# Kernel optimization log

Hardware: AMD Instinct MI355X
Metric: run time of the kernel (lower is better)

The kernel has to match this reference:

```python
import jax, jax.numpy as jnp
import numpy as np

VOCAB = 1024
EMBED_DIM = 64
COMMIT_COST = 0.25


def setup_inputs() -> dict:
    key = jax.random.key(0)
    k1, k2 = jax.random.split(key)
    z_e = jax.random.normal(k1, (64, 64, 32, 32), dtype=jnp.float32)
    # nn.Embedding init: uniform(-1/vocab, 1/vocab)
    embedding = jax.random.uniform(
        k2, (VOCAB, EMBED_DIM), dtype=jnp.float32,
        minval=-1.0 / VOCAB, maxval=1.0 / VOCAB)
    return {"z_e": z_e, "embedding": embedding}


def reference(z_e, embedding):
    b, d, h, w = z_e.shape
    # [B,D,H,W] -> [N,D]
    flat_z = jnp.transpose(z_e, (0, 2, 3, 1)).reshape(-1, d)
    # squared L2 distances to each code: [N, V]
    distances = (
        jnp.sum(flat_z * flat_z, axis=1, keepdims=True)
        + jnp.sum(embedding * embedding, axis=1)
        - 2.0 * flat_z @ embedding.T
    )
    flat_indices = jnp.argmin(distances, axis=1)
    indices = flat_indices.reshape(b, h, w)
    # gather codes and restore [B,D,H,W]
    z_q = embedding[flat_indices].reshape(b, h, w, d)
    z_q = jnp.transpose(z_q, (0, 3, 1, 2))
    quantization_loss = jnp.mean((z_q - jax.lax.stop_gradient(z_e)) ** 2)
    commitment_loss = jnp.mean((z_e - jax.lax.stop_gradient(z_q)) ** 2) * COMMIT_COST
    z_q_st = z_e + jax.lax.stop_gradient(z_q - z_e)
    # perplexity over codebook usage
    counts = jnp.zeros((VOCAB,), dtype=jnp.float32).at[flat_indices].add(1.0)
    avg_probs = counts / flat_indices.shape[0]
    perplexity = jnp.exp(-jnp.sum(avg_probs * jnp.log(avg_probs + 1e-10)))
    return (z_q_st, indices, quantization_loss, commitment_loss, perplexity)
```

## Files before the change

### kernel.cpp

```cpp
#include <hip/hip_runtime.h>
#include <math.h>

#define VOCAB 1024
#define ED 64
#define NROWS 65536
#define NELEM 4194304
#define MARGIN 2.0e-4f
#define CAPF 8192

typedef __attribute__((ext_vector_type(8))) short short8;
typedef __attribute__((ext_vector_type(4))) float f32x4;

__device__ __forceinline__ unsigned f2bf(float f) {
    unsigned u = __float_as_uint(f);
    u += 0x7fff + ((u >> 16) & 1);
    return u >> 16;
}

__device__ __forceinline__ unsigned long long packkey(float d, int c) {
    unsigned f = __float_as_uint(d);
    unsigned sd = (f & 0x80000000u) ? ~f : (f | 0x80000000u);
    return ((unsigned long long)sd << 32) | (unsigned)c;
}


__global__ void vq_prep(const float* __restrict__ emb, float* __restrict__ e2f,
                        uint4* __restrict__ FB, unsigned* __restrict__ zw1,
                        unsigned* __restrict__ zw2) {
    const int tid = blockIdx.x * 256 + threadIdx.x;
    for (int i = tid; i < 1028; i += 2048) zw1[i] = 0u;
    for (int i = tid; i < 3072; i += 2048) zw2[i] = 0u;

    if (tid < VOCAB) {
        const float4* src = (const float4*)(emb + tid * ED);
        double s = 0.0;
        #pragma unroll
        for (int g = 0; g < 16; ++g) {
            float4 f = src[g];
            s = fma((double)f.x, (double)f.x, s);
            s = fma((double)f.y, (double)f.y, s);
            s = fma((double)f.z, (double)f.z, s);
            s = fma((double)f.w, (double)f.w, s);
        }
        e2f[tid] = (float)s;
    }
    #pragma unroll
    for (int e = 0; e < 4; ++e) {
        const int i = e * 2048 + tid;
        const int n = i & 15, q = (i >> 4) & 3, kh = (i >> 6) & 1, T = i >> 7;
        const int code = T * 16 + n;
        const int k0 = kh * 32 + q * 8;
        const float4* sp = (const float4*)(emb + code * 64 + k0);
        float4 f0 = sp[0], f1 = sp[1];
        uint4 pk;
        pk.x = f2bf(f0.x) | (f2bf(f0.y) << 16);
        pk.y = f2bf(f0.z) | (f2bf(f0.w) << 16);
        pk.z = f2bf(f1.x) | (f2bf(f1.y) << 16);
        pk.w = f2bf(f1.z) | (f2bf(f1.w) << 16);
        FB[i] = pk;
    }
}

__global__ __launch_bounds__(256, 2)
void vq_filter(const float* __restrict__ z, const float* __restrict__ emb,
               const float* __restrict__ e2f, const uint4* __restrict__ FB,
               float* __restrict__ out, double* __restrict__ lossp,
               unsigned* __restrict__ hist, unsigned* __restrict__ nflag,
               unsigned* __restrict__ rowlist, float* __restrict__ zrow) {
    __shared__ uint4 Bs4[4096];
    __shared__ float e2s[1024];
    __shared__ float rowb1[128], rowb2[128];
    __shared__ int   rowi1[128], rowfl[128];
    __shared__ double wls[4];

    const int t = threadIdx.x;
    const int w = t >> 6, lane = t & 63;
    const int q = lane >> 4, n_lo = lane & 15;
    const int bk = blockIdx.x;
    const int n0 = bk * 128;
    const int b  = n0 >> 10;
    const int sb = n0 & 1023;

    #pragma unroll
    for (int i = 0; i < 4; ++i) e2s[i * 256 + t] = e2f[i * 256 + t];

    short8 af[2][2];
    #pragma unroll
    for (int rt = 0; rt < 2; ++rt) {
        const int s = sb + w * 32 + rt * 16 + n_lo;
        const float* zp = z + (size_t)b * 65536 + s;
        #pragma unroll
        for (int kh = 0; kh < 2; ++kh) {
            short8 fr;
            #pragma unroll
            for (int j = 0; j < 8; ++j) {
                int d = kh * 32 + q * 8 + j;
                fr[j] = (short)f2bf(-2.0f * zp[d * 1024]);
            }
            af[rt][kh] = fr;
        }
    }

    float b1[8], b2[8]; int i1[8];
    #pragma unroll
    for (int sl = 0; sl < 8; ++sl) { b1[sl] = 3.4e38f; b2[sl] = 3.4e38f; i1[sl] = 0; }

    const short8* FBs = (const short8*)Bs4;
    for (int h = 0; h < 2; ++h) {
        __syncthreads();
        {
            const uint4* src = FB + h * 4096;
            #pragma unroll
            for (int i = 0; i < 16; ++i) Bs4[i * 256 + t] = src[i * 256 + t];
        }
        __syncthreads();
        #pragma unroll 2
        for (int tt = 0; tt < 32; ++tt) {
            const int T = h * 32 + tt;
            short8 bf0 = FBs[tt * 128 + lane];
            short8 bf1 = FBs[tt * 128 + 64 + lane];
            const int cb = T * 16 + n_lo;
            const float e2 = e2s[cb];
            #pragma unroll
            for (int rt = 0; rt < 2; ++rt) {
                f32x4 a; a[0] = e2; a[1] = e2; a[2] = e2; a[3] = e2;
                a = __builtin_amdgcn_mfma_f32_16x16x32_bf16(af[rt][0], bf0, a, 0, 0, 0);
                a = __builtin_amdgcn_mfma_f32_16x16x32_bf16(af[rt][1], bf1, a, 0, 0, 0);
                #pragma unroll
                for (int reg = 0; reg < 4; ++reg) {
                    const int sl = rt * 4 + reg;
                    float s0 = a[reg];
                    b2[sl] = __builtin_amdgcn_fmed3f(s0, b1[sl], b2[sl]);
                    bool lt = s0 < b1[sl];
                    i1[sl] = lt ? cb : i1[sl];
                    b1[sl] = lt ? s0 : b1[sl];
                }
            }
        }
    }

    #pragma unroll
    for (int m = 1; m < 16; m <<= 1) {
        #pragma unroll
        for (int sl = 0; sl < 8; ++sl) {
            float ob1 = __shfl_xor(b1[sl], m, 64);
            int   oi1 = __shfl_xor(i1[sl], m, 64);
            float ob2 = __shfl_xor(b2[sl], m, 64);
            float lose = fmaxf(b1[sl], ob1);
            b2[sl] = fminf(fminf(b2[sl], ob2), lose);
            bool take = (ob1 < b1[sl]) || (ob1 == b1[sl] && oi1 < i1[sl]);
            b1[sl] = take ? ob1 : b1[sl];
            i1[sl] = take ? oi1 : i1[sl];
        }
    }
    if (n_lo == 0) {
        #pragma unroll
        for (int rt = 0; rt < 2; ++rt) {
            #pragma unroll
            for (int reg = 0; reg < 4; ++reg) {
                int row = w * 32 + rt * 16 + q * 4 + reg;
                int sl = rt * 4 + reg;
                rowb1[row] = b1[sl];
                rowb2[row] = b2[sl];
                rowi1[row] = i1[sl];
            }
        }
    }
    __syncthreads();

    if (t < 128) {
        const int nrow = n0 + t;
        const int code = rowi1[t];
        const bool want = rowb2[t] < rowb1[t] + MARGIN;
        unsigned long long mask = __ballot(want);
        const int cnt = __popcll(mask);
        unsigned base = 0;
        if (lane == 0 && cnt > 0) base = atomicAdd(nflag, (unsigned)cnt);
        base = (unsigned)__shfl((int)base, 0, 64);
        int myslot = -1;
        if (want) {
            const int rank = __popcll(mask & ((1ULL << lane) - 1ULL));
            const unsigned slot = base + (unsigned)rank;
            if (slot < CAPF) { rowlist[slot] = (unsigned)nrow; myslot = (int)slot; }
        }
        rowfl[t] = myslot;
        out[NELEM + nrow] = (float)code;
        if (myslot < 0) atomicAdd(&hist[code], 1u);
    }
    __syncthreads();

    {
        const int r = t & 127, tg = t >> 7;
        const int code2 = rowi1[r];
        const int sl2 = rowfl[r];
        const bool fl2 = sl2 >= 0;
        const int scol = sb + r;
        double lsum = 0.0;
        #pragma unroll
        for (int i = 0; i < 8; ++i) {
            const int d4 = tg * 8 + i;
            float4 e4 = *(const float4*)(emb + code2 * 64 + d4 * 4);
            float es[4] = {e4.x, e4.y, e4.z, e4.w};
            #pragma unroll
            for (int j = 0; j < 4; ++j) {
                int d = d4 * 4 + j;
                size_t off = (size_t)b * 65536 + (size_t)d * 1024 + scol;
                float zv = z[off];
                out[off] = zv + (es[j] - zv);
                if (fl2) zrow[(size_t)sl2 * 64 + d] = zv;
                double df = (double)es[j] - (double)zv;
                lsum = fma(df, df, lsum);
            }
        }
        if (fl2) lsum = 0.0;
        #pragma unroll
        for (int off = 32; off > 0; off >>= 1)
            lsum += __shfl_down(lsum, off, 64);
        if (lane == 0) wls[w] = lsum;
    }
    __syncthreads();
    if (t == 0) lossp[bk] = wls[0] + wls[1] + wls[2] + wls[3];
}

#define EDOT(i) { \
    const float4 a4 = za4[i]; \
    const float4 b4 = zb4[i]; \
    ma = fmaf(a4.x, e##i[0], ma); ma = fmaf(a4.y, e##i[1], ma); \
    ma = fmaf(a4.z, e##i[2], ma); ma = fmaf(a4.w, e##i[3], ma); \
    mb = fmaf(b4.x, e##i[0], mb); mb = fmaf(b4.y, e##i[1], mb); \
    mb = fmaf(b4.z, e##i[2], mb); mb = fmaf(b4.w, e##i[3], mb); }

__global__ __launch_bounds__(512, 1)
void vq_rescue(const float* __restrict__ zrow, const float* __restrict__ emb,
               const float* __restrict__ e2f, float* __restrict__ out,
               double* __restrict__ lossp2, unsigned* __restrict__ hist,
               const unsigned* __restrict__ nflag,
               const unsigned* __restrict__ rowlist) {
    __shared__ float zns[16];
    __shared__ unsigned long long wkey[16][16];
    __shared__ int rbi[16];
    __shared__ double lred[8];

    const int t = threadIdx.x, w = t >> 6, lane = t & 63;
    const int g = blockIdx.x;
    unsigned nfr = *nflag;
    const int nf = (int)(nfr < CAPF ? nfr : CAPF);
    if (g * 16 >= nf) return;
    const int nloc = (nf - g * 16 < 16) ? (nf - g * 16) : 16;

    if (t < nloc) {
        const float* zp = zrow + (size_t)(g * 16 + t) * 64;
        double a = 0.0;
        for (int k = 0; k < 64; ++k) { const double v = (double)zp[k]; a = fma(v, v, a); }
        zns[t] = (float)a;
    }
    __syncthreads();

    for (int pass = 0; pass < 2; ++pass) {
        const int cbase = pass * 512 + w * 64;
        const int c = cbase + lane;
        const f32x4* ep = (const f32x4*)(emb + (size_t)c * 64);
        f32x4 e0 = ep[0],  e1 = ep[1],  e2 = ep[2],  e3 = ep[3];
        f32x4 e4 = ep[4],  e5 = ep[5],  e6 = ep[6],  e7 = ep[7];
        f32x4 e8 = ep[8],  e9 = ep[9],  e10 = ep[10], e11 = ep[11];
        f32x4 e12 = ep[12], e13 = ep[13], e14 = ep[14], e15 = ep[15];
        const float e2c = e2f[c];

        for (int r0 = 0; r0 < nloc; r0 += 2) {
            const bool two = (r0 + 1 < nloc);
            const float4* za4 = (const float4*)(zrow + (size_t)(g * 16 + r0) * 64);
            const float4* zb4 = (const float4*)(zrow + (size_t)(g * 16 + (two ? r0 + 1 : r0)) * 64);
            float ma = 0.f, mb = 0.f;
            EDOT(0)  EDOT(1)  EDOT(2)  EDOT(3)
            EDOT(4)  EDOT(5)  EDOT(6)  EDOT(7)
            EDOT(8)  EDOT(9)  EDOT(10) EDOT(11)
            EDOT(12) EDOT(13) EDOT(14) EDOT(15)

            {
                const float da = (zns[r0] + e2c) - 2.0f * ma;
                float dmin = da;
                #pragma unroll
                for (int mo = 32; mo > 0; mo >>= 1)
                    dmin = fminf(dmin, __shfl_xor(dmin, mo, 64));
                const unsigned long long ball = __ballot(da == dmin);
                const int wl = __ffsll(ball) - 1;
                if (lane == 0) wkey[pass * 8 + w][r0] = packkey(dmin, cbase + wl);
            }
            if (two) {
                const float db = (zns[r0 + 1] + e2c) - 2.0f * mb;
                float dmin = db;
                #pragma unroll
                for (int mo = 32; mo > 0; mo >>= 1)
                    dmin = fminf(dmin, __shfl_xor(dmin, mo, 64));
                const unsigned long long ball = __ballot(db == dmin);
                const int wl = __ffsll(ball) - 1;
                if (lane == 0) wkey[pass * 8 + w][r0 + 1] = packkey(dmin, cbase + wl);
            }
        }
    }
    __syncthreads();

    if (t < nloc) {
        unsigned long long k0 = wkey[0][t];
        #pragma unroll
        for (int i = 1; i < 16; ++i) {
            unsigned long long ki = wkey[i][t];
            if (ki < k0) k0 = ki;
        }
        const int code = (int)(unsigned)(k0 & 0xffffffffu);
        rbi[t] = code;
        const int row = (int)rowlist[g * 16 + t];
        out[NELEM + row] = (float)code;
        atomicAdd(&hist[code], 1u);
    }
    __syncthreads();

    double lsum = 0.0;
    if (t < 128) {
        const int r = t >> 3, d0 = (t & 7) * 8;
        if (r < nloc) {
            const int row = (int)rowlist[g * 16 + r];
            const int bb = row >> 10, s = row & 1023;
            const int code = rbi[r];
            float4 ea = *(const float4*)(emb + code * 64 + d0);
            float4 eb = *(const float4*)(emb + code * 64 + d0 + 4);
            float es[8] = {ea.x, ea.y, ea.z, ea.w, eb.x, eb.y, eb.z, eb.w};
            const float* zp = zrow + (size_t)(g * 16 + r) * 64 + d0;
            #pragma unroll
            for (int j = 0; j < 8; ++j) {
                const int d = d0 + j;
                const size_t off = (size_t)bb * 65536 + (size_t)d * 1024 + s;
                const float zv = zp[j];
                out[off] = zv + (es[j] - zv);
                double df = (double)es[j] - (double)zv;
                lsum = fma(df, df, lsum);
            }
        }
    }
    #pragma unroll
    for (int o = 32; o > 0; o >>= 1) lsum += __shfl_down(lsum, o, 64);
    if (lane == 0) lred[w] = lsum;
    __syncthreads();
    if (t == 0) {
        double s = 0.0;
        #pragma unroll
        for (int i = 0; i < 8; ++i) s += lred[i];
        lossp2[g] = s;
    }
}

__global__ void vq_finalize_kernel(const unsigned* __restrict__ hist,
                                   const double* __restrict__ lossp,
                                   const double* __restrict__ lossp2,
                                   float* __restrict__ out) {
    __shared__ double red[256], red2[256];
    int t = threadIdx.x;
    double ssum = 0.0, lsum = 0.0;
    for (int i = t; i < VOCAB; i += 256) {
        double p = (double)hist[i] / (double)NROWS;
        ssum += p * log(p + 1e-10);
    }
    for (int i = t; i < 1024; i += 256) lsum += lossp[i];
    for (int i = t; i < 512; i += 256) lsum += lossp2[i];
    red[t] = ssum; red2[t] = lsum;
    __syncthreads();
    for (int off = 128; off > 0; off >>= 1) {
        if (t < off) { red[t] += red[t + off]; red2[t] += red2[t + off]; }
        __syncthreads();
    }
    if (t == 0) {
        double qv = red2[0] / (double)NELEM;
        out[NELEM + NROWS + 0] = (float)qv;
        out[NELEM + NROWS + 1] = (float)(qv * 0.25);
        out[NELEM + NROWS + 2] = (float)exp(-red[0]);
    }
}

extern "C" void kernel_launch(void* const* d_in, const int* in_sizes, int n_in,
                              void* d_out, int out_size, void* d_ws, size_t ws_size,
                              hipStream_t stream) {
    const float* z   = (const float*)d_in[0];
    const float* emb = (const float*)d_in[1];
    float* out = (float*)d_out;

    float*    e2f     = (float*)d_ws;
    unsigned* nfl     = (unsigned*)((char*)d_ws + 4096);
    unsigned* hist    = (unsigned*)((char*)d_ws + 4112);
    unsigned* rowlist = (unsigned*)((char*)d_ws + 8208);
    uint4*    FB      = (uint4*)((char*)d_ws + 40976);
    double*   lossp   = (double*)((char*)d_ws + 172048);
    double*   lossp2  = (double*)((char*)d_ws + 180240);
    float*    zrow    = (float*)((char*)d_ws + 184336);
    unsigned* zw1     = (unsigned*)((char*)d_ws + 4096);
    unsigned* zw2     = (unsigned*)((char*)d_ws + 172048);

    vq_prep<<<dim3(8), dim3(256), 0, stream>>>(emb, e2f, FB, zw1, zw2);
    vq_filter<<<dim3(512), dim3(256), 0, stream>>>(z, emb, e2f, FB, out, lossp,
                                                   hist, nfl, rowlist, zrow);
    vq_rescue<<<dim3(512), dim3(512), 0, stream>>>(zrow, emb, e2f, out, lossp2,
                                                   hist, nfl, rowlist);
    vq_finalize_kernel<<<dim3(1), dim3(256), 0, stream>>>(hist, lossp, lossp2, out);
}
```

Measured before the change: 158.3 us.

## Split codebook scan across four blocks per row group and merge partial minima

The fused filter kernel is split into two. vq_scan runs 2048 blocks, each scanning a quarter of the codebook for 128 rows, and writes per-row best, second-best and index to workspace. vq_merge then reduces the four partials per row, handles flagging, the histogram, the output write and the loss. This raises parallelism and occupancy, and scan blocks read B fragments straight from global/L2 instead of staging them in LDS. The cost is an extra kernel launch, partial-result traffic, and the z fragments being loaded four times.

```diff
diff --git a/kernel.cpp b/kernel.cpp
--- a/kernel.cpp
+++ b/kernel.cpp
@@ -29,7 +29,7 @@
                         unsigned* __restrict__ zw2) {
     const int tid = blockIdx.x * 256 + threadIdx.x;
     for (int i = tid; i < 1028; i += 2048) zw1[i] = 0u;
-    for (int i = tid; i < 3072; i += 2048) zw2[i] = 0u;
+    for (int i = tid; i < 1536; i += 2048) zw2[i] = 0u;
 
     if (tid < VOCAB) {
         const float4* src = (const float4*)(emb + tid * ED);
@@ -61,28 +61,22 @@
     }
 }
 
-__global__ __launch_bounds__(256, 2)
-void vq_filter(const float* __restrict__ z, const float* __restrict__ emb,
-               const float* __restrict__ e2f, const uint4* __restrict__ FB,
-               float* __restrict__ out, double* __restrict__ lossp,
-               unsigned* __restrict__ hist, unsigned* __restrict__ nflag,
-               unsigned* __restrict__ rowlist, float* __restrict__ zrow) {
-    __shared__ uint4 Bs4[4096];
-    __shared__ float e2s[1024];
-    __shared__ float rowb1[128], rowb2[128];
-    __shared__ int   rowi1[128], rowfl[128];
-    __shared__ double wls[4];
+__global__ __launch_bounds__(256, 4)
+void vq_scan(const float* __restrict__ z, const float* __restrict__ e2f,
+             const uint4* __restrict__ FB, float* __restrict__ pb1,
+             float* __restrict__ pb2, unsigned short* __restrict__ pi1) {
+    __shared__ float e2s[256];
 
     const int t = threadIdx.x;
     const int w = t >> 6, lane = t & 63;
     const int q = lane >> 4, n_lo = lane & 15;
     const int bk = blockIdx.x;
-    const int n0 = bk * 128;
+    const int rg = bk >> 2, ck = bk & 3;
+    const int n0 = rg * 128;
     const int b  = n0 >> 10;
     const int sb = n0 & 1023;
 
-    #pragma unroll
-    for (int i = 0; i < 4; ++i) e2s[i * 256 + t] = e2f[i * 256 + t];
+    if (t < 256) e2s[t] = e2f[ck * 256 + t];
 
     short8 af[2][2];
     #pragma unroll
@@ -105,36 +99,29 @@
     #pragma unroll
     for (int sl = 0; sl < 8; ++sl) { b1[sl] = 3.4e38f; b2[sl] = 3.4e38f; i1[sl] = 0; }
 
-    const short8* FBs = (const short8*)Bs4;
-    for (int h = 0; h < 2; ++h) {
-        __syncthreads();
-        {
-            const uint4* src = FB + h * 4096;
+    __syncthreads();
+
+    const short8* FBs = (const short8*)FB;
+    #pragma unroll 4
+    for (int tt = 0; tt < 16; ++tt) {
+        const int T = ck * 16 + tt;
+        short8 bf0 = FBs[T * 128 + lane];
+        short8 bf1 = FBs[T * 128 + 64 + lane];
+        const int cb = T * 16 + n_lo;
+        const float e2 = e2s[tt * 16 + n_lo];
+        #pragma unroll
+        for (int rt = 0; rt < 2; ++rt) {
+            f32x4 a; a[0] = e2; a[1] = e2; a[2] = e2; a[3] = e2;
+            a = __builtin_amdgcn_mfma_f32_16x16x32_bf16(af[rt][0], bf0, a, 0, 0, 0);
+            a = __builtin_amdgcn_mfma_f32_16x16x32_bf16(af[rt][1], bf1, a, 0, 0, 0);
             #pragma unroll
-            for (int i = 0; i < 16; ++i) Bs4[i * 256 + t] = src[i * 256 + t];
-        }
-        __syncthreads();
-        #pragma unroll 2
-        for (int tt = 0; tt < 32; ++tt) {
-            const int T = h * 32 + tt;
-            short8 bf0 = FBs[tt * 128 + lane];
-            short8 bf1 = FBs[tt * 128 + 64 + lane];
-            const int cb = T * 16 + n_lo;
-            const float e2 = e2s[cb];
-            #pragma unroll
-            for (int rt = 0; rt < 2; ++rt) {
-                f32x4 a; a[0] = e2; a[1] = e2; a[2] = e2; a[3] = e2;
-                a = __builtin_amdgcn_mfma_f32_16x16x32_bf16(af[rt][0], bf0, a, 0, 0, 0);
-                a = __builtin_amdgcn_mfma_f32_16x16x32_bf16(af[rt][1], bf1, a, 0, 0, 0);
-                #pragma unroll
-                for (int reg = 0; reg < 4; ++reg) {
-                    const int sl = rt * 4 + reg;
-                    float s0 = a[reg];
-                    b2[sl] = __builtin_amdgcn_fmed3f(s0, b1[sl], b2[sl]);
-                    bool lt = s0 < b1[sl];
-                    i1[sl] = lt ? cb : i1[sl];
-                    b1[sl] = lt ? s0 : b1[sl];
-                }
+            for (int reg = 0; reg < 4; ++reg) {
+                const int sl = rt * 4 + reg;
+                float s0 = a[reg];
+                b2[sl] = __builtin_amdgcn_fmed3f(s0, b1[sl], b2[sl]);
+                bool lt = s0 < b1[sl];
+                i1[sl] = lt ? cb : i1[sl];
+                b1[sl] = lt ? s0 : b1[sl];
             }
         }
     }
@@ -158,68 +145,85 @@
         for (int rt = 0; rt < 2; ++rt) {
             #pragma unroll
             for (int reg = 0; reg < 4; ++reg) {
-                int row = w * 32 + rt * 16 + q * 4 + reg;
-                int sl = rt * 4 + reg;
-                rowb1[row] = b1[sl];
-                rowb2[row] = b2[sl];
-                rowi1[row] = i1[sl];
-            }
-        }
-    }
-    __syncthreads();
-
-    if (t < 128) {
-        const int nrow = n0 + t;
-        const int code = rowi1[t];
-        const bool want = rowb2[t] < rowb1[t] + MARGIN;
-        unsigned long long mask = __ballot(want);
-        const int cnt = __popcll(mask);
-        unsigned base = 0;
-        if (lane == 0 && cnt > 0) base = atomicAdd(nflag, (unsigned)cnt);
-        base = (unsigned)__shfl((int)base, 0, 64);
-        int myslot = -1;
-        if (want) {
-            const int rank = __popcll(mask & ((1ULL << lane) - 1ULL));
-            const unsigned slot = base + (unsigned)rank;
-            if (slot < CAPF) { rowlist[slot] = (unsigned)nrow; myslot = (int)slot; }
-        }
-        rowfl[t] = myslot;
-        out[NELEM + nrow] = (float)code;
-        if (myslot < 0) atomicAdd(&hist[code], 1u);
-    }
-    __syncthreads();
-
-    {
-        const int r = t & 127, tg = t >> 7;
-        const int code2 = rowi1[r];
-        const int sl2 = rowfl[r];
-        const bool fl2 = sl2 >= 0;
-        const int scol = sb + r;
-        double lsum = 0.0;
-        #pragma unroll
-        for (int i = 0; i < 8; ++i) {
-            const int d4 = tg * 8 + i;
-            float4 e4 = *(const float4*)(emb + code2 * 64 + d4 * 4);
-            float es[4] = {e4.x, e4.y, e4.z, e4.w};
-            #pragma unroll
-            for (int j = 0; j < 4; ++j) {
-                int d = d4 * 4 + j;
-                size_t off = (size_t)b * 65536 + (size_t)d * 1024 + scol;
-                float zv = z[off];
-                out[off] = zv + (es[j] - zv);
-                if (fl2) zrow[(size_t)sl2 * 64 + d] = zv;
-                double df = (double)es[j] - (double)zv;
-                lsum = fma(df, df, lsum);
-            }
-        }
-        if (fl2) lsum = 0.0;
-        #pragma unroll
-        for (int off = 32; off > 0; off >>= 1)
-            lsum += __shfl_down(lsum, off, 64);
-        if (lane == 0) wls[w] = lsum;
-    }
-    __syncthreads();
-    if (t == 0) lossp[bk] = wls[0] + wls[1] + wls[2] + wls[3];
+                const int sl = rt * 4 + reg;
+                const int gr = ck * 65536 + n0 + w * 32 + rt * 16 + q * 4 + reg;
+                pb1[gr] = b1[sl];
+                pb2[gr] = b2[sl];
+                pi1[gr] = (unsigned short)i1[sl];
+            }
+        }
+    }
+}
+
+__global__ __launch_bounds__(256, 2)
+void vq_merge(const float* __restrict__ z, const float* __restrict__ emb,
+              const float* __restrict__ pb1, const float* __restrict__ pb2,
+              const unsigned short* __restrict__ pi1, float* __restrict__ out,
+              double* __restrict__ lossp, unsigned* __restrict__ hist,
+              unsigned* __restrict__ nflag, unsigned* __restrict__ rowlist,
+              float* __restrict__ zrow) {
+    __shared__ unsigned wcnt[4], wpf[4], bshare;
+    __shared__ double wls[4];
+
+    const int t = threadIdx.x, w = t >> 6, lane = t & 63;
+    const int nrow = blockIdx.x * 256 + t;
+    const int b = nrow >> 10, s = nrow & 1023;
+
+    float B1 = pb1[nrow], B2 = pb2[nrow]; int I1 = (int)pi1[nrow];
+    #pragma unroll
+    for (int c = 1; c < 4; ++c) {
+        const float c1 = pb1[c * 65536 + nrow];
+        const float c2 = pb2[c * 65536 + nrow];
+        const int   ci = (int)pi1[c * 65536 + nrow];
+        const float lose = fmaxf(B1, c1);
+        B2 = fminf(fminf(B2, c2), lose);
+        if (c1 < B1) { B1 = c1; I1 = ci; }
+    }
+
+    const bool want = B2 < B1 + MARGIN;
+    const unsigned long long mask = __ballot(want);
+    const int cnt = __popcll(mask);
+    if (lane == 0) wcnt[w] = (unsigned)cnt;
+    __syncthreads();
+    if (t == 0) {
+        const unsigned p0 = wcnt[0], p1 = wcnt[1], p2 = wcnt[2], p3 = wcnt[3];
+        const unsigned tot = p0 + p1 + p2 + p3;
+        bshare = tot ? atomicAdd(nflag, tot) : 0u;
+        wpf[0] = 0; wpf[1] = p0; wpf[2] = p0 + p1; wpf[3] = p0 + p1 + p2;
+    }
+    __syncthreads();
+    int myslot = -1;
+    if (want) {
+        const int rank = __popcll(mask & ((1ULL << lane) - 1ULL));
+        const unsigned slot = bshare + wpf[w] + (unsigned)rank;
+        if (slot < CAPF) { rowlist[slot] = (unsigned)nrow; myslot = (int)slot; }
+    }
+    out[NELEM + nrow] = (float)I1;
+    if (myslot < 0) atomicAdd(&hist[I1], 1u);
+
+    double l0 = 0.0, l1 = 0.0;
+    const float4* em4 = (const float4*)(emb + I1 * 64);
+    #pragma unroll
+    for (int d4 = 0; d4 < 16; ++d4) {
+        const float4 e4 = em4[d4];
+        const float es[4] = {e4.x, e4.y, e4.z, e4.w};
+        #pragma unroll
+        for (int j = 0; j < 4; ++j) {
+            const int d = d4 * 4 + j;
+            const size_t off = (size_t)b * 65536 + (size_t)d * 1024 + s;
+            const float zv = z[off];
+            out[off] = zv + (es[j] - zv);
+            if (myslot >= 0) zrow[(size_t)myslot * 64 + d] = zv;
+            const double df = (double)es[j] - (double)zv;
+            if (j & 1) l1 = fma(df, df, l1); else l0 = fma(df, df, l0);
+        }
+    }
+    double lsum = (myslot >= 0) ? 0.0 : (l0 + l1);
+    #pragma unroll
+    for (int o = 32; o > 0; o >>= 1) lsum += __shfl_down(lsum, o, 64);
+    if (lane == 0) wls[w] = lsum;
+    __syncthreads();
+    if (t == 0) lossp[blockIdx.x] = wls[0] + wls[1] + wls[2] + wls[3];
 }
 
 #define EDOT(i) { \
@@ -360,7 +364,7 @@
         double p = (double)hist[i] / (double)NROWS;
         ssum += p * log(p + 1e-10);
     }
-    for (int i = t; i < 1024; i += 256) lsum += lossp[i];
+    lsum += lossp[t];
     for (int i = t; i < 512; i += 256) lsum += lossp2[i];
     red[t] = ssum; red2[t] = lsum;
     __syncthreads();
@@ -383,20 +387,24 @@
     const float* emb = (const float*)d_in[1];
     float* out = (float*)d_out;
 
-    float*    e2f     = (float*)d_ws;
-    unsigned* nfl     = (unsigned*)((char*)d_ws + 4096);
-    unsigned* hist    = (unsigned*)((char*)d_ws + 4112);
-    unsigned* rowlist = (unsigned*)((char*)d_ws + 8208);
-    uint4*    FB      = (uint4*)((char*)d_ws + 40976);
-    double*   lossp   = (double*)((char*)d_ws + 172048);
-    double*   lossp2  = (double*)((char*)d_ws + 180240);
-    float*    zrow    = (float*)((char*)d_ws + 184336);
-    unsigned* zw1     = (unsigned*)((char*)d_ws + 4096);
-    unsigned* zw2     = (unsigned*)((char*)d_ws + 172048);
+    float*          e2f     = (float*)d_ws;
+    unsigned*       nfl     = (unsigned*)((char*)d_ws + 4096);
+    unsigned*       hist    = (unsigned*)((char*)d_ws + 4112);
+    unsigned*       rowlist = (unsigned*)((char*)d_ws + 8208);
+    uint4*          FB      = (uint4*)((char*)d_ws + 40976);
+    double*         lossp   = (double*)((char*)d_ws + 172048);
+    double*         lossp2  = (double*)((char*)d_ws + 174096);
+    float*          pb1     = (float*)((char*)d_ws + 178192);
+    float*          pb2     = (float*)((char*)d_ws + 1226768);
+    unsigned short* pi1     = (unsigned short*)((char*)d_ws + 2275344);
+    float*          zrow    = (float*)((char*)d_ws + 2799632);
+    unsigned*       zw1     = (unsigned*)((char*)d_ws + 4096);
+    unsigned*       zw2     = (unsigned*)((char*)d_ws + 172048);
 
     vq_prep<<<dim3(8), dim3(256), 0, stream>>>(emb, e2f, FB, zw1, zw2);
-    vq_filter<<<dim3(512), dim3(256), 0, stream>>>(z, emb, e2f, FB, out, lossp,
-                                                   hist, nfl, rowlist, zrow);
+    vq_scan<<<dim3(2048), dim3(256), 0, stream>>>(z, e2f, FB, pb1, pb2, pi1);
+    vq_merge<<<dim3(256), dim3(256), 0, stream>>>(z, emb, pb1, pb2, pi1, out,
+                                                  lossp, hist, nfl, rowlist, zrow);
     vq_rescue<<<dim3(512), dim3(512), 0, stream>>>(zrow, emb, e2f, out, lossp2,
                                                    hist, nfl, rowlist);
     vq_finalize_kernel<<<dim3(1), dim3(256), 0, stream>>>(hist, lossp, lossp2, out);
```

New measurement: 174.6 us. 10.3% more time.
